# Performance work log

Measured on AMD Instinct MI355X. Metric: run time of the kernel, lower is better.

## Reference

```python
import jax, jax.numpy as jnp
import numpy as np

H = 8        # heads
DH = 64      # dim_head
EPS = 1e-5   # LayerNorm eps (torch default)


def setup_inputs() -> dict:
    key = jax.random.key(0)
    k0, k1, k2, k3, k4 = jax.random.split(key, 5)
    b, l, n, dim = 2, 8, 256, 512
    inner = H * DH
    return {
        "xyzs": jax.random.normal(k0, (b, l, n, 3), dtype=jnp.float32),
        "features": jax.random.normal(k1, (b, l, n, dim), dtype=jnp.float32),
        "ln_gamma": jnp.ones((dim,), dtype=jnp.float32),
        "ln_beta": jnp.zeros((dim,), dtype=jnp.float32),
        "w_qkv": jax.random.normal(k2, (dim, 3 * inner), dtype=jnp.float32) * 0.02,
        "w_sp": jax.random.normal(k3, (3, DH), dtype=jnp.float32) * 0.3,
        "w_out": jax.random.normal(k4, (inner, dim), dtype=jnp.float32) * 0.02,
        "b_out": jnp.zeros((dim,), dtype=jnp.float32),
    }


def reference(xyzs, features, ln_gamma, ln_beta, w_qkv, w_sp, w_out, b_out):
    b, l, n, dim = features.shape
    m = l * n
    inner = H * DH
    scale = DH ** (-0.5)

    # LayerNorm over last dim (biased variance, eps=1e-5)
    mu = jnp.mean(features, axis=-1, keepdims=True)
    var = jnp.var(features, axis=-1, keepdims=True)
    normed = (features - mu) * jax.lax.rsqrt(var + EPS) * ln_gamma + ln_beta

    # qkv projection, chunk into q,k,v, reshape 'b l n (h d) -> b h (l n) d'
    qkv = normed.reshape(b, m, dim) @ w_qkv            # [b, m, 3*inner]
    def split_heads(t):
        return t.reshape(b, m, H, DH).transpose(0, 2, 1, 3)  # [b, h, m, d]
    q = split_heads(qkv[..., :inner])
    k = split_heads(qkv[..., inner:2 * inner])
    v = split_heads(qkv[..., 2 * inner:])

    dots = jnp.einsum('bhid,bhjd->bhij', q, k) * scale  # [b, h, m, m]
    attn = jax.nn.softmax(dots, axis=-1)
    v_out = jnp.einsum('bhij,bhjd->bhid', attn, v)      # [b, h, m, d]

    # pairwise coordinate deltas: delta[b,i,j,c] = xyz[b,j,c] - xyz[b,i,c]
    xyz_f = xyzs.reshape(b, m, 3)
    delta = xyz_f[:, None, :, :] - xyz_f[:, :, None, :]  # [b, m, m, 3]
    # attention-weighted aggregation over j (avoids [b,h,m,m,3] intermediate)
    agg = jnp.einsum('bhij,bijc->bhic', attn, delta)     # [b, h, m, 3]
    disp = agg @ w_sp                                    # [b, h, m, DH]

    out = v_out + disp                                   # [b, h, m, DH]
    out = out.transpose(0, 2, 1, 3).reshape(b, m, inner) # 'b h m d -> b m (h d)'
    out = jax.nn.gelu(out @ w_out + b_out, approximate=False)
    return out.reshape(b, l, n, dim) + features
```

## Files before the change

### kernel.cpp

```cpp
#include <hip/hip_runtime.h>
#include <hip/hip_bf16.h>
#include <math.h>

#define BB   2
#define MM   2048
#define DIM  512
#define NH   8
#define DHd  64
#define NQK  1536
#define ROWS 4096
#define NROW 32768
#define SPLITK 4

typedef __hip_bfloat16 bf16;
typedef __attribute__((ext_vector_type(8))) short bf16x8;
typedef __attribute__((ext_vector_type(4))) float f32x4;
typedef __attribute__((ext_vector_type(8))) unsigned short us8;

__device__ __forceinline__ unsigned short f2bf_bits(float x) {
    bf16 h = __float2bfloat16(x);
    return *(unsigned short*)&h;
}
__device__ __forceinline__ float bf2f(unsigned short u) {
    unsigned int v = ((unsigned int)u) << 16;
    return __uint_as_float(v);
}

__global__ __launch_bounds__(256) void pre_kernel(
    const float* __restrict__ feat, const float* __restrict__ gamma,
    const float* __restrict__ beta, unsigned short* __restrict__ normed,
    const float* __restrict__ wqkv, const float* __restrict__ wout,
    unsigned short* __restrict__ wqkvT, unsigned short* __restrict__ woutT)
{
    __shared__ float st[64][65];
    int b = blockIdx.x;
    int tid = threadIdx.x;
    if (b < ROWS / 4) {
        int w = tid >> 6, lane = tid & 63;
        int row = b * 4 + w;
        const float* fr = feat + (size_t)row * DIM + lane * 8;
        float4 v0 = *(const float4*)fr;
        float4 v1 = *(const float4*)(fr + 4);
        float s  = v0.x + v0.y + v0.z + v0.w + v1.x + v1.y + v1.z + v1.w;
        float ss = v0.x*v0.x + v0.y*v0.y + v0.z*v0.z + v0.w*v0.w
                 + v1.x*v1.x + v1.y*v1.y + v1.z*v1.z + v1.w*v1.w;
        #pragma unroll
        for (int o = 32; o >= 1; o >>= 1) { s += __shfl_xor(s, o); ss += __shfl_xor(ss, o); }
        float mu  = s * (1.0f / DIM);
        float var = ss * (1.0f / DIM) - mu * mu;
        float inv = rsqrtf(var + 1e-5f);
        const float* gp = gamma + lane * 8;
        const float* bp = beta  + lane * 8;
        float4 g0 = *(const float4*)gp, g1 = *(const float4*)(gp + 4);
        float4 e0 = *(const float4*)bp, e1 = *(const float4*)(bp + 4);
        unsigned short ov[8];
        ov[0] = f2bf_bits((v0.x - mu) * inv * g0.x + e0.x);
        ov[1] = f2bf_bits((v0.y - mu) * inv * g0.y + e0.y);
        ov[2] = f2bf_bits((v0.z - mu) * inv * g0.z + e0.z);
        ov[3] = f2bf_bits((v0.w - mu) * inv * g0.w + e0.w);
        ov[4] = f2bf_bits((v1.x - mu) * inv * g1.x + e1.x);
        ov[5] = f2bf_bits((v1.y - mu) * inv * g1.y + e1.y);
        ov[6] = f2bf_bits((v1.z - mu) * inv * g1.z + e1.z);
        ov[7] = f2bf_bits((v1.w - mu) * inv * g1.w + e1.w);
        *(us8*)&normed[(size_t)row * DIM + lane * 8] = *(us8*)ov;
        return;
    }
    int idx = b - ROWS / 4;
    const float* in; unsigned short* out; int N, n0;
    if (idx < 192) { in = wqkv; out = wqkvT; N = NQK; n0 = (idx >> 3) * 64; }
    else { idx -= 192; in = wout; out = woutT; N = DIM; n0 = (idx >> 3) * 64; }
    int k0 = (idx & 7) * 64;
    #pragma unroll
    for (int p = 0; p < 16; p++) {
        int e = tid + p * 256;
        int r = e >> 6, c = e & 63;
        st[r][c] = in[(size_t)(k0 + r) * N + n0 + c];
    }
    __syncthreads();
    #pragma unroll
    for (int p = 0; p < 16; p++) {
        int e = tid + p * 256;
        int nr = e >> 6, kc = e & 63;
        out[(size_t)(n0 + nr) * DIM + k0 + kc] = f2bf_bits(st[kc][nr]);
    }
}

__global__ __launch_bounds__(256) void qkv_gemm(
    const unsigned short* __restrict__ A, const unsigned short* __restrict__ BT,
    unsigned short* __restrict__ qd, unsigned short* __restrict__ kd,
    unsigned short* __restrict__ vd)
{
    __shared__ __align__(16) unsigned short sA[128 * 72];
    __shared__ __align__(16) unsigned short sB[64 * 72];
    int tid = threadIdx.x;
    int r0 = blockIdx.x * 128;
    int n0 = blockIdx.y * 64;
    int chunk = n0 >> 9;
    int h     = (n0 & 511) >> 6;
    int w = tid >> 6, lane = tid & 63;
    int wm = w >> 1, wn = w & 1;
    int ln15 = lane & 15, quad = lane >> 4;

    int arow = tid >> 1, acol = (tid & 1) * 32;
    int brow = tid >> 2, bcol = (tid & 3) * 16;

    f32x4 acc[4][2] = {};
    us8 ra[4], rb[2];

    #pragma unroll
    for (int u = 0; u < 4; u++)
        ra[u] = *(const us8*)&A[(size_t)(r0 + arow) * DIM + acol + u * 8];
    #pragma unroll
    for (int u = 0; u < 2; u++)
        rb[u] = *(const us8*)&BT[(size_t)(n0 + brow) * DIM + bcol + u * 8];

    for (int k0 = 0; k0 < DIM; k0 += 64) {
        __syncthreads();
        #pragma unroll
        for (int u = 0; u < 4; u++) *(us8*)&sA[arow * 72 + acol + u * 8] = ra[u];
        #pragma unroll
        for (int u = 0; u < 2; u++) *(us8*)&sB[brow * 72 + bcol + u * 8] = rb[u];
        __syncthreads();
        int kn = k0 + 64;
        if (kn < DIM) {
            #pragma unroll
            for (int u = 0; u < 4; u++)
                ra[u] = *(const us8*)&A[(size_t)(r0 + arow) * DIM + kn + acol + u * 8];
            #pragma unroll
            for (int u = 0; u < 2; u++)
                rb[u] = *(const us8*)&BT[(size_t)(n0 + brow) * DIM + kn + bcol + u * 8];
        }
        bf16x8 fa[4][2], fb[2][2];
        #pragma unroll
        for (int i = 0; i < 4; i++)
            #pragma unroll
            for (int kk = 0; kk < 2; kk++)
                fa[i][kk] = *(const bf16x8*)&sA[(wm * 64 + i * 16 + ln15) * 72 + kk * 32 + quad * 8];
        #pragma unroll
        for (int j = 0; j < 2; j++)
            #pragma unroll
            for (int kk = 0; kk < 2; kk++)
                fb[j][kk] = *(const bf16x8*)&sB[(wn * 32 + j * 16 + ln15) * 72 + kk * 32 + quad * 8];
        if (chunk == 2) {
            #pragma unroll
            for (int kk = 0; kk < 2; kk++)
                #pragma unroll
                for (int i = 0; i < 4; i++)
                    #pragma unroll
                    for (int j = 0; j < 2; j++)
                        acc[i][j] = __builtin_amdgcn_mfma_f32_16x16x32_bf16(fa[i][kk], fb[j][kk], acc[i][j], 0, 0, 0);
        } else {
            #pragma unroll
            for (int kk = 0; kk < 2; kk++)
                #pragma unroll
                for (int i = 0; i < 4; i++)
                    #pragma unroll
                    for (int j = 0; j < 2; j++)
                        acc[i][j] = __builtin_amdgcn_mfma_f32_16x16x32_bf16(fb[j][kk], fa[i][kk], acc[i][j], 0, 0, 0);
        }
    }

    if (chunk == 2) {
        #pragma unroll
        for (int i = 0; i < 4; i++) {
            int gm = r0 + wm * 64 + i * 16 + quad * 4;
            int bb = gm >> 11, mm = gm & 2047;
            #pragma unroll
            for (int j = 0; j < 2; j++) {
                int d = wn * 32 + j * 16 + ln15;
                ushort4 pk;
                pk.x = f2bf_bits(acc[i][j][0]);
                pk.y = f2bf_bits(acc[i][j][1]);
                pk.z = f2bf_bits(acc[i][j][2]);
                pk.w = f2bf_bits(acc[i][j][3]);
                *(ushort4*)&vd[((size_t)(bb * NH + h) * DHd + d) * MM + mm] = pk;
            }
        }
    } else {
        unsigned short* dst = (chunk == 0) ? qd : kd;
        float sc = (chunk == 0) ? 0.125f : 1.0f;
        #pragma unroll
        for (int i = 0; i < 4; i++) {
            int gm = r0 + wm * 64 + i * 16 + ln15;
            int bb = gm >> 11, mm = gm & 2047;
            #pragma unroll
            for (int j = 0; j < 2; j++) {
                int d0 = wn * 32 + j * 16 + quad * 4;
                ushort4 pk;
                pk.x = f2bf_bits(acc[i][j][0] * sc);
                pk.y = f2bf_bits(acc[i][j][1] * sc);
                pk.z = f2bf_bits(acc[i][j][2] * sc);
                pk.w = f2bf_bits(acc[i][j][3] * sc);
                *(ushort4*)&dst[((size_t)(bb * NH + h) * MM + mm) * DHd + d0] = pk;
            }
        }
    }
}

__global__ __launch_bounds__(256, 4) void attn_kernel(
    const unsigned short* __restrict__ qg, const unsigned short* __restrict__ kg,
    const unsigned short* __restrict__ vg, const float* __restrict__ xyzs,
    unsigned short* __restrict__ obuf, float* __restrict__ lbuf)
{
    __shared__ __align__(16) unsigned short sK[64 * 72];
    __shared__ __align__(16) unsigned short sVT[80 * 72];
    __shared__ __align__(16) unsigned short sP[128 * 72];

    int tid = threadIdx.x;
    int bh = blockIdx.y; int bb = bh >> 3;
    int i0 = blockIdx.x * 128;
    int ks = blockIdx.z;
    int w = tid >> 6;
    int lane = tid & 63;
    int ln15 = lane & 15;
    int quad = lane >> 4;

    for (int e = tid; e < 12 * 72; e += 256) sVT[68 * 72 + e] = 0;
    if (tid < 64) sVT[67 * 72 + tid] = 0x3F80;

    bf16x8 aq[2][2];
    {
        const unsigned short* q0 = qg + ((size_t)bh * MM + i0 + w * 32 + ln15) * DHd + quad * 8;
        aq[0][0] = *(const bf16x8*)q0;
        aq[0][1] = *(const bf16x8*)(q0 + 32);
        aq[1][0] = *(const bf16x8*)(q0 + 16 * DHd);
        aq[1][1] = *(const bf16x8*)(q0 + 16 * DHd + 32);
    }

    f32x4 o[2][5] = {};

    const unsigned short* kbase = kg + (size_t)bh * MM * DHd;
    const unsigned short* vbase = vg + (size_t)bh * DHd * MM;
    int jbeg = ks * (MM / SPLITK), jend = jbeg + (MM / SPLITK);

    int srow = tid >> 2, scol16 = (tid & 3) * 16;

    us8 rk0, rk1, rv0, rv1;
    float rx = 0.f;
    {
        const unsigned short* src = kbase + (size_t)jbeg * DHd;
        rk0 = *(const us8*)&src[(size_t)tid * 16];
        rk1 = *(const us8*)&src[(size_t)tid * 16 + 8];
        const unsigned short* vs = vbase + jbeg;
        rv0 = *(const us8*)&vs[(size_t)srow * MM + scol16];
        rv1 = *(const us8*)&vs[(size_t)srow * MM + scol16 + 8];
        if (tid < 192) rx = xyzs[((size_t)bb * MM + jbeg) * 3 + tid];
    }

    int pwb = quad << 4;
    int swzr = (ln15 >> 2) << 4;
    int pr0 = (quad * 8) ^ swzr;
    int pr1 = (32 + quad * 8) ^ swzr;

    for (int jt = jbeg; jt < jend; jt += 64) {
        __syncthreads();
        *(us8*)&sK[srow * 72 + scol16]      = rk0;
        *(us8*)&sK[srow * 72 + scol16 + 8]  = rk1;
        *(us8*)&sVT[srow * 72 + scol16]     = rv0;
        *(us8*)&sVT[srow * 72 + scol16 + 8] = rv1;
        if (tid < 192) {
            int key = tid / 3, c = tid - key * 3;
            sVT[(64 + c) * 72 + key] = f2bf_bits(rx);
        }
        __syncthreads();
        int jn = jt + 64;
        if (jn < jend) {
            const unsigned short* src = kbase + (size_t)jn * DHd;
            rk0 = *(const us8*)&src[(size_t)tid * 16];
            rk1 = *(const us8*)&src[(size_t)tid * 16 + 8];
            const unsigned short* vs = vbase + jn;
            rv0 = *(const us8*)&vs[(size_t)srow * MM + scol16];
            rv1 = *(const us8*)&vs[(size_t)srow * MM + scol16 + 8];
            if (tid < 192) rx = xyzs[((size_t)bb * MM + jn) * 3 + tid];
        }

        #pragma unroll
        for (int t = 0; t < 4; t++) {
            bf16x8 bk0 = *(const bf16x8*)&sK[(t * 16 + ln15) * 72 + quad * 8];
            bf16x8 bk1 = *(const bf16x8*)&sK[(t * 16 + ln15) * 72 + 32 + quad * 8];
            int colb = (t * 16) ^ pwb;
            #pragma unroll
            for (int rf = 0; rf < 2; rf++) {
                f32x4 z = {};
                z = __builtin_amdgcn_mfma_f32_16x16x32_bf16(aq[rf][0], bk0, z, 0, 0, 0);
                z = __builtin_amdgcn_mfma_f32_16x16x32_bf16(aq[rf][1], bk1, z, 0, 0, 0);
                int rbase = (w * 32 + rf * 16 + quad * 4) * 72 + colb + ln15;
                sP[rbase]           = f2bf_bits(__expf(z[0]));
                sP[rbase + 72]      = f2bf_bits(__expf(z[1]));
                sP[rbase + 144]     = f2bf_bits(__expf(z[2]));
                sP[rbase + 216]     = f2bf_bits(__expf(z[3]));
            }
        }
        asm volatile("s_waitcnt lgkmcnt(0)" ::: "memory");
        bf16x8 ap[2][2];
        ap[0][0] = *(const bf16x8*)&sP[(w * 32 + ln15) * 72 + pr0];
        ap[0][1] = *(const bf16x8*)&sP[(w * 32 + ln15) * 72 + pr1];
        ap[1][0] = *(const bf16x8*)&sP[(w * 32 + 16 + ln15) * 72 + pr0];
        ap[1][1] = *(const bf16x8*)&sP[(w * 32 + 16 + ln15) * 72 + pr1];
        #pragma unroll
        for (int t = 0; t < 5; t++) {
            bf16x8 bv0 = *(const bf16x8*)&sVT[(t * 16 + ln15) * 72 + quad * 8];
            bf16x8 bv1 = *(const bf16x8*)&sVT[(t * 16 + ln15) * 72 + 32 + quad * 8];
            #pragma unroll
            for (int rf = 0; rf < 2; rf++) {
                o[rf][t] = __builtin_amdgcn_mfma_f32_16x16x32_bf16(ap[rf][0], bv0, o[rf][t], 0, 0, 0);
                o[rf][t] = __builtin_amdgcn_mfma_f32_16x16x32_bf16(ap[rf][1], bv1, o[rf][t], 0, 0, 0);
            }
        }
    }

    size_t kso = (size_t)ks * NROW;
    #pragma unroll
    for (int rf = 0; rf < 2; rf++) {
        #pragma unroll
        for (int reg = 0; reg < 4; reg++) {
            size_t row = (size_t)bh * MM + i0 + w * 32 + rf * 16 + quad * 4 + reg;
            unsigned short* orow = obuf + (kso + row) * 72;
            #pragma unroll
            for (int t = 0; t < 4; t++)
                orow[t * 16 + ln15] = f2bf_bits(o[rf][t][reg]);
            if (ln15 < 3)  orow[64 + ln15] = f2bf_bits(o[rf][4][reg]);
            if (ln15 == 3) lbuf[kso + row] = o[rf][4][reg];
        }
    }
}

__global__ __launch_bounds__(256) void merge_kernel(
    const unsigned short* __restrict__ obuf, const float* __restrict__ lbuf,
    const float* __restrict__ xyzs, const float* __restrict__ wsp,
    unsigned short* __restrict__ attn_out)
{
    __shared__ float sW[3][64];
    int tid = threadIdx.x;
    if (tid < 192) sW[tid >> 6][tid & 63] = wsp[tid];
    __syncthreads();
    int r   = blockIdx.x * 64 + (tid >> 2);
    int d0  = (tid & 3) * 16;
    int bh = r >> 11, qrow = r & 2047, bb = bh >> 3, hh = bh & 7;
    const unsigned short* p0 = obuf + (size_t)r * 72;
    const unsigned short* p1 = p0 + (size_t)NROW * 72;
    const unsigned short* p2 = p1 + (size_t)NROW * 72;
    const unsigned short* p3 = p2 + (size_t)NROW * 72;
    float invl = 1.f / (lbuf[r] + lbuf[NROW + r] + lbuf[2 * NROW + r] + lbuf[3 * NROW + r]);
    size_t xb = ((size_t)bb * MM + qrow) * 3;
    float gx = (bf2f(p0[64]) + bf2f(p1[64]) + bf2f(p2[64]) + bf2f(p3[64])) * invl - xyzs[xb + 0];
    float gy = (bf2f(p0[65]) + bf2f(p1[65]) + bf2f(p2[65]) + bf2f(p3[65])) * invl - xyzs[xb + 1];
    float gz = (bf2f(p0[66]) + bf2f(p1[66]) + bf2f(p2[66]) + bf2f(p3[66])) * invl - xyzs[xb + 2];
    us8 a0 = *(const us8*)&p0[d0];
    us8 a1 = *(const us8*)&p0[d0 + 8];
    us8 b0 = *(const us8*)&p1[d0];
    us8 b1 = *(const us8*)&p1[d0 + 8];
    us8 c0 = *(const us8*)&p2[d0];
    us8 c1 = *(const us8*)&p2[d0 + 8];
    us8 e0 = *(const us8*)&p3[d0];
    us8 e1 = *(const us8*)&p3[d0 + 8];
    unsigned short outv[16];
    #pragma unroll
    for (int e = 0; e < 8; e++) {
        int d = d0 + e;
        float v = (bf2f(a0[e]) + bf2f(b0[e]) + bf2f(c0[e]) + bf2f(e0[e])) * invl
                + gx * sW[0][d] + gy * sW[1][d] + gz * sW[2][d];
        outv[e] = f2bf_bits(v);
    }
    #pragma unroll
    for (int e = 0; e < 8; e++) {
        int d = d0 + 8 + e;
        float v = (bf2f(a1[e]) + bf2f(b1[e]) + bf2f(c1[e]) + bf2f(e1[e])) * invl
                + gx * sW[0][d] + gy * sW[1][d] + gz * sW[2][d];
        outv[8 + e] = f2bf_bits(v);
    }
    unsigned short* dst = attn_out + ((size_t)bb * MM + qrow) * DIM + hh * DHd + d0;
    *(us8*)dst       = *(us8*)&outv[0];
    *(us8*)(dst + 8) = *(us8*)&outv[8];
}

__global__ __launch_bounds__(256) void out_gemm(
    const unsigned short* __restrict__ A, const unsigned short* __restrict__ BT,
    const float* __restrict__ bias, const float* __restrict__ feat,
    float* __restrict__ out)
{
    __shared__ __align__(16) unsigned short sA[64 * 72];
    __shared__ __align__(16) unsigned short sB[64 * 72];
    int tid = threadIdx.x;
    int r0 = blockIdx.x * 64, n0 = blockIdx.y * 64;
    int w = tid >> 6, lane = tid & 63;
    int wm = w >> 1, wn = w & 1;
    int ln15 = lane & 15, quad = lane >> 4;

    int srow = tid >> 2, scol = (tid & 3) * 16;

    f32x4 acc[2][2] = {};
    us8 ra[2], rb[2];

    #pragma unroll
    for (int u = 0; u < 2; u++) {
        ra[u] = *(const us8*)&A[(size_t)(r0 + srow) * DIM + scol + u * 8];
        rb[u] = *(const us8*)&BT[(size_t)(n0 + srow) * DIM + scol + u * 8];
    }

    for (int k0 = 0; k0 < DIM; k0 += 64) {
        __syncthreads();
        #pragma unroll
        for (int u = 0; u < 2; u++) {
            *(us8*)&sA[srow * 72 + scol + u * 8] = ra[u];
            *(us8*)&sB[srow * 72 + scol + u * 8] = rb[u];
        }
        __syncthreads();
        int kn = k0 + 64;
        if (kn < DIM) {
            #pragma unroll
            for (int u = 0; u < 2; u++) {
                ra[u] = *(const us8*)&A[(size_t)(r0 + srow) * DIM + kn + scol + u * 8];
                rb[u] = *(const us8*)&BT[(size_t)(n0 + srow) * DIM + kn + scol + u * 8];
            }
        }
        bf16x8 af[2][2], bf_[2][2];
        #pragma unroll
        for (int i = 0; i < 2; i++)
            #pragma unroll
            for (int kk = 0; kk < 2; kk++)
                af[i][kk] = *(const bf16x8*)&sA[(wm * 32 + i * 16 + ln15) * 72 + kk * 32 + quad * 8];
        #pragma unroll
        for (int j = 0; j < 2; j++)
            #pragma unroll
            for (int kk = 0; kk < 2; kk++)
                bf_[j][kk] = *(const bf16x8*)&sB[(wn * 32 + j * 16 + ln15) * 72 + kk * 32 + quad * 8];
        #pragma unroll
        for (int kk = 0; kk < 2; kk++)
            #pragma unroll
            for (int i = 0; i < 2; i++)
                #pragma unroll
                for (int j = 0; j < 2; j++)
                    acc[i][j] = __builtin_amdgcn_mfma_f32_16x16x32_bf16(af[i][kk], bf_[j][kk], acc[i][j], 0, 0, 0);
    }

    #pragma unroll
    for (int i = 0; i < 2; i++) {
        #pragma unroll
        for (int reg = 0; reg < 4; reg++) {
            int gr = r0 + wm * 32 + i * 16 + quad * 4 + reg;
            #pragma unroll
            for (int j = 0; j < 2; j++) {
                int c = n0 + wn * 32 + j * 16 + ln15;
                float x = acc[i][j][reg] + bias[c];
                float g = 0.5f * x * (1.f + erff(x * 0.70710678118f));
                out[(size_t)gr * DIM + c] = g + feat[(size_t)gr * DIM + c];
            }
        }
    }
}

extern "C" void kernel_launch(void* const* d_in, const int* in_sizes, int n_in,
                              void* d_out, int out_size, void* d_ws, size_t ws_size,
                              hipStream_t stream)
{
    const float* xyzs  = (const float*)d_in[0];
    const float* feat  = (const float*)d_in[1];
    const float* gamma = (const float*)d_in[2];
    const float* beta  = (const float*)d_in[3];
    const float* wqkv  = (const float*)d_in[4];
    const float* wsp   = (const float*)d_in[5];
    const float* wout  = (const float*)d_in[6];
    const float* bout  = (const float*)d_in[7];
    float* out = (float*)d_out;

    unsigned short* ws16 = (unsigned short*)d_ws;
    const size_t SEGS = (size_t)ROWS * DIM;
    unsigned short* normed = ws16;
    unsigned short* qb     = ws16 + SEGS;
    unsigned short* kb     = ws16 + 2 * SEGS;
    unsigned short* vb     = ws16 + 3 * SEGS;
    unsigned short* wqkvT  = ws16 + 4 * SEGS;
    unsigned short* woutT  = wqkvT + (size_t)NQK * DIM;
    unsigned short* obuf   = woutT + (size_t)DIM * DIM;
    float*          lbuf   = (float*)(obuf + (size_t)SPLITK * NROW * 72);

    pre_kernel<<<ROWS / 4 + 256, 256, 0, stream>>>(feat, gamma, beta, normed,
                                                   wqkv, wout, wqkvT, woutT);
    qkv_gemm<<<dim3(32, 24), 256, 0, stream>>>(normed, wqkvT, qb, kb, vb);
    attn_kernel<<<dim3(16, 16, SPLITK), 256, 0, stream>>>(qb, kb, vb, xyzs, obuf, lbuf);
    merge_kernel<<<512, 256, 0, stream>>>(obuf, lbuf, xyzs, wsp, normed);
    out_gemm<<<dim3(64, 8), 256, 0, stream>>>(normed, woutT, bout, feat, out);
}
```

Baseline: 144.1 us.

## Switch attention to 32x32 MFMA with register-resident P via permlane swaps

The attention kernel moves from 16x16x32 to 32x32x16 bf16 MFMA and computes S transposed (K as the A operand), so the exponentiated scores can be packed to bf16 and reshuffled in registers with v_permlane32_swap. This feeds them directly into the PV MFMA instead of round-tripping through an sP shared-memory buffer. It also changes the key split from 4 to 3 uneven chunks (704/704/640), trims the merge kernel to three partials, and lowers launch-bound occupancy to 3. The cost is extra register pressure from 16-wide accumulators and a padded V/xyz tile (96 rows) that wastes some MFMA work on zero rows.

Measured after the change: 141.8 us. No clear change (-1.6%).

```diff
diff --git a/kernel.cpp b/kernel.cpp
--- a/kernel.cpp
+++ b/kernel.cpp
@@ -10,12 +10,14 @@
 #define NQK  1536
 #define ROWS 4096
 #define NROW 32768
-#define SPLITK 4
+#define SPLITK 3
 
 typedef __hip_bfloat16 bf16;
 typedef __attribute__((ext_vector_type(8))) short bf16x8;
 typedef __attribute__((ext_vector_type(4))) float f32x4;
+typedef __attribute__((ext_vector_type(16))) float f32x16;
 typedef __attribute__((ext_vector_type(8))) unsigned short us8;
+typedef __attribute__((ext_vector_type(4))) unsigned int u32x4;
 
 __device__ __forceinline__ unsigned short f2bf_bits(float x) {
     bf16 h = __float2bfloat16(x);
@@ -24,6 +26,14 @@
 __device__ __forceinline__ float bf2f(unsigned short u) {
     unsigned int v = ((unsigned int)u) << 16;
     return __uint_as_float(v);
+}
+__device__ __forceinline__ unsigned cvtpk_bf16(float lo, float hi) {
+    unsigned r;
+    asm("v_cvt_pk_bf16_f32 %0, %1, %2" : "=v"(r) : "v"(lo), "v"(hi));
+    return r;
+}
+__device__ __forceinline__ void pl32swap(unsigned &a, unsigned &b) {
+    asm volatile("v_permlane32_swap_b32 %0, %1" : "+v"(a), "+v"(b));
 }
 
 __global__ __launch_bounds__(256) void pre_kernel(
@@ -197,14 +207,13 @@
     }
 }
 
-__global__ __launch_bounds__(256, 4) void attn_kernel(
+__global__ __launch_bounds__(256, 3) void attn_kernel(
     const unsigned short* __restrict__ qg, const unsigned short* __restrict__ kg,
     const unsigned short* __restrict__ vg, const float* __restrict__ xyzs,
     unsigned short* __restrict__ obuf, float* __restrict__ lbuf)
 {
     __shared__ __align__(16) unsigned short sK[64 * 72];
-    __shared__ __align__(16) unsigned short sVT[80 * 72];
-    __shared__ __align__(16) unsigned short sP[128 * 72];
+    __shared__ __align__(16) unsigned short sVT[96 * 72];
 
     int tid = threadIdx.x;
     int bh = blockIdx.y; int bb = bh >> 3;
@@ -212,26 +221,27 @@
     int ks = blockIdx.z;
     int w = tid >> 6;
     int lane = tid & 63;
-    int ln15 = lane & 15;
-    int quad = lane >> 4;
-
-    for (int e = tid; e < 12 * 72; e += 256) sVT[68 * 72 + e] = 0;
+    int ln31 = lane & 31;
+    int hi   = lane >> 5;
+    int hi8  = hi * 8;
+
+    for (int e = tid; e < 28 * 72; e += 256) sVT[68 * 72 + e] = 0;
     if (tid < 64) sVT[67 * 72 + tid] = 0x3F80;
 
-    bf16x8 aq[2][2];
+    bf16x8 aq[4];
     {
-        const unsigned short* q0 = qg + ((size_t)bh * MM + i0 + w * 32 + ln15) * DHd + quad * 8;
-        aq[0][0] = *(const bf16x8*)q0;
-        aq[0][1] = *(const bf16x8*)(q0 + 32);
-        aq[1][0] = *(const bf16x8*)(q0 + 16 * DHd);
-        aq[1][1] = *(const bf16x8*)(q0 + 16 * DHd + 32);
-    }
-
-    f32x4 o[2][5] = {};
+        const unsigned short* q0 = qg + ((size_t)bh * MM + i0 + w * 32 + ln31) * DHd + hi8;
+        #pragma unroll
+        for (int kc = 0; kc < 4; kc++)
+            aq[kc] = *(const bf16x8*)(q0 + kc * 16);
+    }
+
+    f32x16 ot[3] = {};
 
     const unsigned short* kbase = kg + (size_t)bh * MM * DHd;
     const unsigned short* vbase = vg + (size_t)bh * DHd * MM;
-    int jbeg = ks * (MM / SPLITK), jend = jbeg + (MM / SPLITK);
+    int jbeg = ks * 704;
+    int jend = (ks == 2) ? MM : jbeg + 704;
 
     int srow = tid >> 2, scol16 = (tid & 3) * 16;
 
@@ -247,11 +257,6 @@
         if (tid < 192) rx = xyzs[((size_t)bb * MM + jbeg) * 3 + tid];
     }
 
-    int pwb = quad << 4;
-    int swzr = (ln15 >> 2) << 4;
-    int pr0 = (quad * 8) ^ swzr;
-    int pr1 = (32 + quad * 8) ^ swzr;
-
     for (int jt = jbeg; jt < jend; jt += 64) {
         __syncthreads();
         *(us8*)&sK[srow * 72 + scol16]      = rk0;
@@ -275,53 +280,55 @@
         }
 
         #pragma unroll
-        for (int t = 0; t < 4; t++) {
-            bf16x8 bk0 = *(const bf16x8*)&sK[(t * 16 + ln15) * 72 + quad * 8];
-            bf16x8 bk1 = *(const bf16x8*)&sK[(t * 16 + ln15) * 72 + 32 + quad * 8];
-            int colb = (t * 16) ^ pwb;
-            #pragma unroll
-            for (int rf = 0; rf < 2; rf++) {
-                f32x4 z = {};
-                z = __builtin_amdgcn_mfma_f32_16x16x32_bf16(aq[rf][0], bk0, z, 0, 0, 0);
-                z = __builtin_amdgcn_mfma_f32_16x16x32_bf16(aq[rf][1], bk1, z, 0, 0, 0);
-                int rbase = (w * 32 + rf * 16 + quad * 4) * 72 + colb + ln15;
-                sP[rbase]           = f2bf_bits(__expf(z[0]));
-                sP[rbase + 72]      = f2bf_bits(__expf(z[1]));
-                sP[rbase + 144]     = f2bf_bits(__expf(z[2]));
-                sP[rbase + 216]     = f2bf_bits(__expf(z[3]));
-            }
-        }
-        asm volatile("s_waitcnt lgkmcnt(0)" ::: "memory");
-        bf16x8 ap[2][2];
-        ap[0][0] = *(const bf16x8*)&sP[(w * 32 + ln15) * 72 + pr0];
-        ap[0][1] = *(const bf16x8*)&sP[(w * 32 + ln15) * 72 + pr1];
-        ap[1][0] = *(const bf16x8*)&sP[(w * 32 + 16 + ln15) * 72 + pr0];
-        ap[1][1] = *(const bf16x8*)&sP[(w * 32 + 16 + ln15) * 72 + pr1];
-        #pragma unroll
-        for (int t = 0; t < 5; t++) {
-            bf16x8 bv0 = *(const bf16x8*)&sVT[(t * 16 + ln15) * 72 + quad * 8];
-            bf16x8 bv1 = *(const bf16x8*)&sVT[(t * 16 + ln15) * 72 + 32 + quad * 8];
-            #pragma unroll
-            for (int rf = 0; rf < 2; rf++) {
-                o[rf][t] = __builtin_amdgcn_mfma_f32_16x16x32_bf16(ap[rf][0], bv0, o[rf][t], 0, 0, 0);
-                o[rf][t] = __builtin_amdgcn_mfma_f32_16x16x32_bf16(ap[rf][1], bv1, o[rf][t], 0, 0, 0);
+        for (int b = 0; b < 2; b++) {
+            f32x16 zz = {};
+            #pragma unroll
+            for (int kc = 0; kc < 4; kc++) {
+                bf16x8 kf = *(const bf16x8*)&sK[(b * 32 + ln31) * 72 + kc * 16 + hi8];
+                zz = __builtin_amdgcn_mfma_f32_32x32x16_bf16(kf, aq[kc], zz, 0, 0, 0);
+            }
+            unsigned c_[8];
+            #pragma unroll
+            for (int j = 0; j < 8; j++)
+                c_[j] = cvtpk_bf16(__expf(zz[2 * j]), __expf(zz[2 * j + 1]));
+            unsigned x0 = c_[0], x2 = c_[2]; pl32swap(x0, x2);
+            unsigned x1 = c_[1], x3 = c_[3]; pl32swap(x1, x3);
+            unsigned y0 = c_[4], y2 = c_[6]; pl32swap(y0, y2);
+            unsigned y1 = c_[5], y3 = c_[7]; pl32swap(y1, y3);
+            u32x4 xv = {x0, x1, x2, x3};
+            u32x4 yv = {y0, y1, y2, y3};
+            bf16x8 X = *(bf16x8*)&xv;
+            bf16x8 Y = *(bf16x8*)&yv;
+            #pragma unroll
+            for (int vb = 0; vb < 3; vb++) {
+                bf16x8 v0 = *(const bf16x8*)&sVT[(vb * 32 + ln31) * 72 + b * 32 + hi8];
+                bf16x8 v1 = *(const bf16x8*)&sVT[(vb * 32 + ln31) * 72 + b * 32 + 16 + hi8];
+                ot[vb] = __builtin_amdgcn_mfma_f32_32x32x16_bf16(v0, X, ot[vb], 0, 0, 0);
+                ot[vb] = __builtin_amdgcn_mfma_f32_32x32x16_bf16(v1, Y, ot[vb], 0, 0, 0);
             }
         }
     }
 
     size_t kso = (size_t)ks * NROW;
-    #pragma unroll
-    for (int rf = 0; rf < 2; rf++) {
-        #pragma unroll
-        for (int reg = 0; reg < 4; reg++) {
-            size_t row = (size_t)bh * MM + i0 + w * 32 + rf * 16 + quad * 4 + reg;
-            unsigned short* orow = obuf + (kso + row) * 72;
-            #pragma unroll
-            for (int t = 0; t < 4; t++)
-                orow[t * 16 + ln15] = f2bf_bits(o[rf][t][reg]);
-            if (ln15 < 3)  orow[64 + ln15] = f2bf_bits(o[rf][4][reg]);
-            if (ln15 == 3) lbuf[kso + row] = o[rf][4][reg];
-        }
+    size_t row = (size_t)bh * MM + i0 + w * 32 + ln31;
+    unsigned short* orow = obuf + (kso + row) * 72;
+    #pragma unroll
+    for (int vb = 0; vb < 2; vb++) {
+        #pragma unroll
+        for (int rq = 0; rq < 4; rq++) {
+            ushort4 pk;
+            pk.x = f2bf_bits(ot[vb][rq * 4 + 0]);
+            pk.y = f2bf_bits(ot[vb][rq * 4 + 1]);
+            pk.z = f2bf_bits(ot[vb][rq * 4 + 2]);
+            pk.w = f2bf_bits(ot[vb][rq * 4 + 3]);
+            *(ushort4*)&orow[vb * 32 + rq * 8 + hi * 4] = pk;
+        }
+    }
+    if (hi == 0) {
+        orow[64] = f2bf_bits(ot[2][0]);
+        orow[65] = f2bf_bits(ot[2][1]);
+        orow[66] = f2bf_bits(ot[2][2]);
+        lbuf[kso + row] = ot[2][3];
     }
 }
 
@@ -340,32 +347,29 @@
     const unsigned short* p0 = obuf + (size_t)r * 72;
     const unsigned short* p1 = p0 + (size_t)NROW * 72;
     const unsigned short* p2 = p1 + (size_t)NROW * 72;
-    const unsigned short* p3 = p2 + (size_t)NROW * 72;
-    float invl = 1.f / (lbuf[r] + lbuf[NROW + r] + lbuf[2 * NROW + r] + lbuf[3 * NROW + r]);
+    float invl = 1.f / (lbuf[r] + lbuf[NROW + r] + lbuf[2 * NROW + r]);
     size_t xb = ((size_t)bb * MM + qrow) * 3;
-    float gx = (bf2f(p0[64]) + bf2f(p1[64]) + bf2f(p2[64]) + bf2f(p3[64])) * invl - xyzs[xb + 0];
-    float gy = (bf2f(p0[65]) + bf2f(p1[65]) + bf2f(p2[65]) + bf2f(p3[65])) * invl - xyzs[xb + 1];
-    float gz = (bf2f(p0[66]) + bf2f(p1[66]) + bf2f(p2[66]) + bf2f(p3[66])) * invl - xyzs[xb + 2];
+    float gx = (bf2f(p0[64]) + bf2f(p1[64]) + bf2f(p2[64])) * invl - xyzs[xb + 0];
+    float gy = (bf2f(p0[65]) + bf2f(p1[65]) + bf2f(p2[65])) * invl - xyzs[xb + 1];
+    float gz = (bf2f(p0[66]) + bf2f(p1[66]) + bf2f(p2[66])) * invl - xyzs[xb + 2];
     us8 a0 = *(const us8*)&p0[d0];
     us8 a1 = *(const us8*)&p0[d0 + 8];
     us8 b0 = *(const us8*)&p1[d0];
     us8 b1 = *(const us8*)&p1[d0 + 8];
     us8 c0 = *(const us8*)&p2[d0];
     us8 c1 = *(const us8*)&p2[d0 + 8];
-    us8 e0 = *(const us8*)&p3[d0];
-    us8 e1 = *(const us8*)&p3[d0 + 8];
     unsigned short outv[16];
     #pragma unroll
     for (int e = 0; e < 8; e++) {
         int d = d0 + e;
-        float v = (bf2f(a0[e]) + bf2f(b0[e]) + bf2f(c0[e]) + bf2f(e0[e])) * invl
+        float v = (bf2f(a0[e]) + bf2f(b0[e]) + bf2f(c0[e])) * invl
                 + gx * sW[0][d] + gy * sW[1][d] + gz * sW[2][d];
         outv[e] = f2bf_bits(v);
     }
     #pragma unroll
     for (int e = 0; e < 8; e++) {
         int d = d0 + 8 + e;
-        float v = (bf2f(a1[e]) + bf2f(b1[e]) + bf2f(c1[e]) + bf2f(e1[e])) * invl
+        float v = (bf2f(a1[e]) + bf2f(b1[e]) + bf2f(c1[e])) * invl
                 + gx * sW[0][d] + gy * sW[1][d] + gz * sW[2][d];
         outv[8 + e] = f2bf_bits(v);
     }
```
